# Kernel tuning notes

Measured on AMD Instinct MI355X. Metric: run time of the kernel, lower is better.

The kernel has to match this reference:

```python
import jax, jax.numpy as jnp
import numpy as np
from jax import lax

D = 1024      # input_dim
H = 4096      # hidden_dim (4*D)
E = 8         # num_experts
TOPK = 2      # sparse_top_k


def setup_inputs() -> dict:
    key = jax.random.key(0)
    ks = jax.random.split(key, 7)
    s = 0.02
    return {
        "x": jax.random.normal(ks[0], (2, 2048, D), dtype=jnp.float32),
        "W1": jax.random.normal(ks[1], (E, D, H), dtype=jnp.float32) * s,
        "b1": jnp.zeros((E, H), dtype=jnp.float32),
        "W2": jax.random.normal(ks[2], (E, H, D), dtype=jnp.float32) * s,
        "b2": jnp.zeros((E, D), dtype=jnp.float32),
        "Wr": jax.random.normal(ks[3], (D, E), dtype=jnp.float32) * s,
        "br": jnp.zeros((E,), dtype=jnp.float32),
    }


def reference(x, W1, b1, W2, b2, Wr, br):
    B, S, _ = x.shape
    xf = x.reshape(-1, D)                                  # [T, D]
    logits = xf @ Wr + br                                  # [T, E]
    # top-k threshold masking (keep logits >= k-th largest, else -inf)
    topv, _ = lax.top_k(logits, TOPK)                      # [T, k]
    thresh = topv[:, TOPK - 1:TOPK]                        # [T, 1]
    masked = jnp.where(logits >= thresh, logits, -jnp.inf)
    weights = jax.nn.softmax(masked, axis=-1)              # [T, E]
    # run ALL experts densely (faithful to reference), then weighted sum
    h = jax.nn.gelu(jnp.einsum('td,edh->eth', xf, W1) + b1[:, None, :],
                    approximate=False)                     # [E, T, H]
    expert_out = jnp.einsum('eth,ehd->etd', h, W2) + b2[:, None, :]  # [E, T, D]
    out = jnp.einsum('etd,te->td', expert_out, weights)    # [T, D]
    return out.reshape(B, S, D)
```

## Files before the change

### kernel.cpp

```cpp
#include <hip/hip_runtime.h>
#include <math.h>

typedef __bf16 bf16x8 __attribute__((ext_vector_type(8)));
typedef float f32x4 __attribute__((ext_vector_type(4)));

#define DDIM 1024
#define HDIM 4096
#define NE 8
#define TT 4096
#define CAP 9216

static const size_t OFF_CTRL   = 0;
static const size_t OFF_ROWMAP = 256;
static const size_t OFF_WROW   = OFF_ROWMAP + (size_t)CAP * 4;
static const size_t OFF_ROWPOS = OFF_WROW + (size_t)CAP * 4;
static const size_t OFF_TOKE   = OFF_ROWPOS + (size_t)TT * 2 * 4;
static const size_t OFF_TOKW   = OFF_TOKE + (size_t)TT * 2 * 4;
static const size_t OFF_XB     = OFF_TOKW + (size_t)TT * 2 * 4;
static const size_t OFF_W1T    = OFF_XB + (size_t)TT * DDIM * 2;
static const size_t OFF_W2T    = OFF_W1T + (size_t)NE * HDIM * DDIM * 2;
static const size_t OFF_H      = OFF_W2T + (size_t)NE * DDIM * HDIM * 2;
static const size_t OFF_PO     = OFF_H + (size_t)CAP * HDIM * 2;
static const size_t WS_NEED    = OFF_PO + (size_t)CAP * DDIM * 4;

__device__ __forceinline__ unsigned short f2bf(float f) {
  unsigned int u = __builtin_bit_cast(unsigned int, f);
  u = (u + 0x7FFFu + ((u >> 16) & 1u)) >> 16;
  return (unsigned short)u;
}

__device__ __forceinline__ void async16(void* lds, const void* g) {
  __builtin_amdgcn_global_load_lds(
      (__attribute__((address_space(1))) void*)g,
      (__attribute__((address_space(3))) void*)lds, 16, 0, 0);
}

__device__ __forceinline__ float gelu_exact(float v) {
  return 0.5f * v * (1.0f + erff(v * 0.70710678118654752f));
}

__global__ __launch_bounds__(256) void router_k(
    const float* __restrict__ x, const float* __restrict__ Wr, const float* __restrict__ br,
    unsigned short* __restrict__ xb, int* __restrict__ toke, float* __restrict__ tokw) {
  int tid = threadIdx.x, lane = tid & 63, wid = tid >> 6;
  int t = blockIdx.x * 4 + wid;
  const float* xr = x + (size_t)t * DDIM;
  float acc[NE];
#pragma unroll
  for (int e = 0; e < NE; ++e) acc[e] = 0.f;
#pragma unroll
  for (int it = 0; it < DDIM / 64; ++it) {
    int d = lane + it * 64;
    float xv = xr[d];
    xb[(size_t)t * DDIM + d] = f2bf(xv);
    const float4* w4 = (const float4*)(Wr + (size_t)d * NE);
    float4 wa = w4[0], wb = w4[1];
    acc[0] += xv * wa.x; acc[1] += xv * wa.y; acc[2] += xv * wa.z; acc[3] += xv * wa.w;
    acc[4] += xv * wb.x; acc[5] += xv * wb.y; acc[6] += xv * wb.z; acc[7] += xv * wb.w;
  }
#pragma unroll
  for (int e = 0; e < NE; ++e) {
#pragma unroll
    for (int s = 32; s > 0; s >>= 1) acc[e] += __shfl_xor(acc[e], s, 64);
  }
  if (lane == 0) {
    float l[NE];
#pragma unroll
    for (int e = 0; e < NE; ++e) l[e] = acc[e] + br[e];
    int i0 = 0; float m0 = l[0];
#pragma unroll
    for (int e = 1; e < NE; ++e) if (l[e] > m0) { m0 = l[e]; i0 = e; }
    int i1 = -1; float m1 = -3.4e38f;
#pragma unroll
    for (int e = 0; e < NE; ++e) if (e != i0 && l[e] > m1) { m1 = l[e]; i1 = e; }
    float e1 = expf(m1 - m0);
    float s = 1.f + e1;
    toke[2 * t] = i0;  toke[2 * t + 1] = i1;
    tokw[2 * t] = 1.f / s;  tokw[2 * t + 1] = e1 / s;
  }
}

__global__ __launch_bounds__(1024) void bin_k(
    const int* __restrict__ toke, const float* __restrict__ tokw,
    int* __restrict__ ctrl, int* __restrict__ rowmap,
    float* __restrict__ wrow, int* __restrict__ rowpos) {
  __shared__ int wcnt[16][8];
  __shared__ int wpre[16][8];
  __shared__ int pbase[9];
  __shared__ int ecnt[8];
  __shared__ int ebase[8];
  int tid = threadIdx.x, lane = tid & 63, w = tid >> 6;

  int myCnt = 0;
  for (int c = 0; c < 8; ++c) {
    int e = toke[c * 1024 + tid];
#pragma unroll
    for (int ee = 0; ee < 8; ++ee) {
      unsigned long long m = __ballot(e == ee);
      if (lane == ee) myCnt += (int)__popcll(m);
    }
  }
  if (lane < 8) wcnt[w][lane] = myCnt;
  __syncthreads();
  if (tid == 0) {
    int off = 0;
    for (int e = 0; e < 8; ++e) {
      int s = 0;
      for (int ww = 0; ww < 16; ++ww) s += wcnt[ww][e];
      ecnt[e] = s;
      pbase[e] = off;
      ebase[e] = off;
      ctrl[8 + e] = off;
      off += ((s + 127) >> 7) << 7;
    }
    pbase[8] = off;
    ctrl[16] = off;
  }
  __syncthreads();

  for (int e = 0; e < 8; ++e) {
    int start = pbase[e] + ecnt[e], end = pbase[e + 1];
    for (int r = start + tid; r < end; r += 1024) { rowmap[r] = 0; wrow[r] = 0.f; }
  }

  for (int c = 0; c < 8; ++c) {
    int slot = c * 1024 + tid;
    int e = toke[slot];
    unsigned long long mown = 0;
#pragma unroll
    for (int ee = 0; ee < 8; ++ee) {
      unsigned long long m = __ballot(e == ee);
      if (lane == ee) wcnt[w][ee] = (int)__popcll(m);
      if (e == ee) mown = m;
    }
    __syncthreads();
    if (tid < 128) {
      int ww = tid >> 3, ee = tid & 7;
      int s = 0;
      for (int p = 0; p < ww; ++p) s += wcnt[p][ee];
      wpre[ww][ee] = s;
    }
    __syncthreads();
    int rank = (int)__popcll(mown & ((1ull << lane) - 1ull));
    int r = ebase[e] + wpre[w][e] + rank;
    rowmap[r] = slot >> 1;
    wrow[r] = tokw[slot];
    rowpos[slot] = r;
    __syncthreads();
    if (tid < 8) {
      int s = 0;
      for (int ww = 0; ww < 16; ++ww) s += wcnt[ww][tid];
      ebase[tid] += s;
    }
    __syncthreads();
  }
}

__global__ __launch_bounds__(256) void convT_k(
    const float* __restrict__ src, unsigned short* __restrict__ dst, int K_, int N_) {
  __shared__ unsigned int lds32[64][33];
  int e = blockIdx.z;
  int kb = blockIdx.y << 6, nb = blockIdx.x << 6;
  int t = threadIdx.x;
  const float* s = src + (size_t)e * K_ * N_ + (size_t)kb * N_ + nb;
  int n0 = (t & 15) << 2;
#pragma unroll
  for (int i = 0; i < 2; ++i) {
    int k2 = (i << 4) + (t >> 4);
    float4 a = *(const float4*)(s + (size_t)(2 * k2) * N_ + n0);
    float4 b = *(const float4*)(s + (size_t)(2 * k2 + 1) * N_ + n0);
    lds32[n0 + 0][k2] = (unsigned)f2bf(a.x) | ((unsigned)f2bf(b.x) << 16);
    lds32[n0 + 1][k2] = (unsigned)f2bf(a.y) | ((unsigned)f2bf(b.y) << 16);
    lds32[n0 + 2][k2] = (unsigned)f2bf(a.z) | ((unsigned)f2bf(b.z) << 16);
    lds32[n0 + 3][k2] = (unsigned)f2bf(a.w) | ((unsigned)f2bf(b.w) << 16);
  }
  __syncthreads();
  unsigned short* dp = dst + (size_t)e * (size_t)N_ * K_ + (size_t)nb * K_ + kb;
  int n = t >> 2, c = t & 3;
  uint4 v0, v1;
  v0.x = lds32[n][(c << 2) + 0]; v0.y = lds32[n][(c << 2) + 1];
  v0.z = lds32[n][(c << 2) + 2]; v0.w = lds32[n][(c << 2) + 3];
  int c4 = (c + 4) << 2;
  v1.x = lds32[n][c4 + 0]; v1.y = lds32[n][c4 + 1];
  v1.z = lds32[n][c4 + 2]; v1.w = lds32[n][c4 + 3];
  *(uint4*)(dp + (size_t)n * K_ + (c << 3)) = v0;
  *(uint4*)(dp + (size_t)n * K_ + ((c + 4) << 3)) = v1;
}

template <int KTOT, int NTOT, bool GATHER, bool DOGELU, bool KSPLIT2>
__global__ __launch_bounds__(256, 2) void gemm_k(
    const unsigned short* __restrict__ A, const unsigned short* __restrict__ Bt,
    const int* __restrict__ ctrl, const int* __restrict__ rowmap,
    const float* __restrict__ wrow, const float* __restrict__ bias,
    unsigned short* __restrict__ outb, float* __restrict__ outf0, float* __restrict__ outf1) {
  __shared__ __align__(16) unsigned short Asm[128 * 64];
  __shared__ __align__(16) unsigned short Bsm[128 * 64];
  int zz = blockIdx.z;
  int e = KSPLIT2 ? (zz & 7) : zz;
  int ks = KSPLIT2 ? (zz >> 3) : 0;
  int off0 = ctrl[8 + e], off1 = ctrl[8 + e + 1];
  int row0 = off0 + (blockIdx.y << 7);
  if (row0 >= off1) return;
  int col0 = blockIdx.x << 7;
  int tid = threadIdx.x, lane = tid & 63, wid = tid >> 6;
  int wr = wid >> 1, wc = wid & 1;
  int kbeg = KSPLIT2 ? ks * (KTOT / 2) : 0;
  int kend = KSPLIT2 ? kbeg + (KTOT / 2) : KTOT;
  float* outf = (KSPLIT2 && ks) ? outf1 : outf0;

  const unsigned short* Asrc[4];
  const unsigned short* Bsrc[4];
#pragma unroll
  for (int c = 0; c < 4; ++c) {
    int ar = row0 + (c << 5) + (tid >> 3);
    size_t arow = GATHER ? (size_t)rowmap[ar] : (size_t)ar;
    Asrc[c] = A + arow * KTOT + ((tid & 7) << 3);
    int brw = col0 + (c << 5) + (tid >> 3);
    Bsrc[c] = Bt + ((size_t)e * NTOT + brw) * KTOT + ((tid & 7) << 3);
  }

  f32x4 acc[4][4];
#pragma unroll
  for (int m = 0; m < 4; ++m)
#pragma unroll
    for (int n = 0; n < 4; ++n) acc[m][n] = (f32x4){0.f, 0.f, 0.f, 0.f};

  int arow_rd = ((wr << 6) + (lane & 15)) << 6;
  int brow_rd = ((wc << 6) + (lane & 15)) << 6;
  int koff = (lane >> 4) << 3;
  char* AsmB = (char*)Asm;
  char* BsmB = (char*)Bsm;

  for (int k0 = kbeg; k0 < kend; k0 += 64) {
#pragma unroll
    for (int c = 0; c < 4; ++c) {
      async16(AsmB + ((c << 8) + (wid << 6)) * 16, Asrc[c] + k0);
      async16(BsmB + ((c << 8) + (wid << 6)) * 16, Bsrc[c] + k0);
    }
    __syncthreads();
#pragma unroll
    for (int kk = 0; kk < 64; kk += 32) {
      bf16x8 af[4], bfr[4];
#pragma unroll
      for (int m = 0; m < 4; ++m)
        af[m] = *(const bf16x8*)&Asm[arow_rd + (m << 10) + kk + koff];
#pragma unroll
      for (int n = 0; n < 4; ++n)
        bfr[n] = *(const bf16x8*)&Bsm[brow_rd + (n << 10) + kk + koff];
#pragma unroll
      for (int m = 0; m < 4; ++m)
#pragma unroll
        for (int n = 0; n < 4; ++n)
          acc[m][n] = __builtin_amdgcn_mfma_f32_16x16x32_bf16(af[m], bfr[n], acc[m][n], 0, 0, 0);
    }
    __syncthreads();
  }

  int r_b = (lane >> 4) << 2;
  int c_b = lane & 15;
  if (DOGELU) {
#pragma unroll
    for (int n = 0; n < 4; ++n) {
      int col = col0 + (wc << 6) + (n << 4) + c_b;
      float bv = bias[e * NTOT + col];
#pragma unroll
      for (int m = 0; m < 4; ++m) {
#pragma unroll
        for (int r = 0; r < 4; ++r) {
          int row = row0 + (wr << 6) + (m << 4) + r_b + r;
          outb[(size_t)row * NTOT + col] = f2bf(gelu_exact(acc[m][n][r] + bv));
        }
      }
    }
  } else {
#pragma unroll
    for (int n = 0; n < 4; ++n) {
      int col = col0 + (wc << 6) + (n << 4) + c_b;
      float bv = (KSPLIT2 && ks) ? 0.f : bias[e * NTOT + col];
#pragma unroll
      for (int m = 0; m < 4; ++m) {
#pragma unroll
        for (int r = 0; r < 4; ++r) {
          int row = row0 + (wr << 6) + (m << 4) + r_b + r;
          outf[(size_t)row * NTOT + col] = wrow[row] * (acc[m][n][r] + bv);
        }
      }
    }
  }
}

__global__ __launch_bounds__(256) void gather_k(
    const float* __restrict__ p0, const float* __restrict__ p1,
    const int* __restrict__ rowpos, float* __restrict__ out) {
  int t = blockIdx.x, d = threadIdx.x << 2;
  int r0 = rowpos[2 * t], r1 = rowpos[2 * t + 1];
  float4 a0 = *(const float4*)&p0[(size_t)r0 * DDIM + d];
  float4 a1 = *(const float4*)&p1[(size_t)r0 * DDIM + d];
  float4 b0 = *(const float4*)&p0[(size_t)r1 * DDIM + d];
  float4 b1 = *(const float4*)&p1[(size_t)r1 * DDIM + d];
  float4 o;
  o.x = (a0.x + a1.x) + (b0.x + b1.x);
  o.y = (a0.y + a1.y) + (b0.y + b1.y);
  o.z = (a0.z + a1.z) + (b0.z + b1.z);
  o.w = (a0.w + a1.w) + (b0.w + b1.w);
  *(float4*)&out[(size_t)t * DDIM + d] = o;
}

extern "C" void kernel_launch(void* const* d_in, const int* in_sizes, int n_in,
                              void* d_out, int out_size, void* d_ws, size_t ws_size,
                              hipStream_t stream) {
  const float* x  = (const float*)d_in[0];
  const float* W1 = (const float*)d_in[1];
  const float* b1 = (const float*)d_in[2];
  const float* W2 = (const float*)d_in[3];
  const float* b2 = (const float*)d_in[4];
  const float* Wr = (const float*)d_in[5];
  const float* br = (const float*)d_in[6];
  float* out = (float*)d_out;

  if (ws_size < WS_NEED) return;

  char* ws = (char*)d_ws;
  int* ctrl            = (int*)(ws + OFF_CTRL);
  int* rowmap          = (int*)(ws + OFF_ROWMAP);
  float* wrow          = (float*)(ws + OFF_WROW);
  int* rowpos          = (int*)(ws + OFF_ROWPOS);
  int* toke            = (int*)(ws + OFF_TOKE);
  float* tokw          = (float*)(ws + OFF_TOKW);
  unsigned short* xb   = (unsigned short*)(ws + OFF_XB);
  unsigned short* W1T  = (unsigned short*)(ws + OFF_W1T);
  unsigned short* W2T  = (unsigned short*)(ws + OFF_W2T);
  unsigned short* hbuf = (unsigned short*)(ws + OFF_H);
  float* pout          = (float*)(ws + OFF_PO);
  float* pout2         = (float*)(ws + OFF_W1T);

  router_k<<<TT / 4, 256, 0, stream>>>(x, Wr, br, xb, toke, tokw);
  bin_k<<<1, 1024, 0, stream>>>(toke, tokw, ctrl, rowmap, wrow, rowpos);

  convT_k<<<dim3(HDIM / 64, DDIM / 64, NE), 256, 0, stream>>>(W1, W1T, DDIM, HDIM);
  convT_k<<<dim3(DDIM / 64, HDIM / 64, NE), 256, 0, stream>>>(W2, W2T, HDIM, DDIM);

  gemm_k<DDIM, HDIM, true, true, false><<<dim3(HDIM / 128, 32, NE), 256, 0, stream>>>(
      xb, W1T, ctrl, rowmap, wrow, b1, hbuf, nullptr, nullptr);
  gemm_k<HDIM, DDIM, false, false, true><<<dim3(DDIM / 128, 32, NE * 2), 256, 0, stream>>>(
      hbuf, W2T, ctrl, rowmap, wrow, b2, nullptr, pout, pout2);

  gather_k<<<TT, 256, 0, stream>>>(pout, pout2, rowpos, out);
}
```

Baseline: 377.7 us.

## Store split-K partial outputs in bf16, vectorize router, raise GEMM occupancy

The second GEMM now writes its split-K partial outputs as bf16 instead of fp32, and the gather kernel converts them back to float before summing. This halves the partial-output write and read traffic and shrinks the workspace. The router loads x as float4 and stores bf16 x as ushort4, and the GEMM launch bound is raised to 4 blocks per CU, which may cap registers and cause spills. Rounding the partials to bf16 before the final sum adds precision loss.

```diff
diff --git a/kernel.cpp b/kernel.cpp
--- a/kernel.cpp
+++ b/kernel.cpp
@@ -21,12 +21,16 @@
 static const size_t OFF_W2T    = OFF_W1T + (size_t)NE * HDIM * DDIM * 2;
 static const size_t OFF_H      = OFF_W2T + (size_t)NE * DDIM * HDIM * 2;
 static const size_t OFF_PO     = OFF_H + (size_t)CAP * HDIM * 2;
-static const size_t WS_NEED    = OFF_PO + (size_t)CAP * DDIM * 4;
+static const size_t WS_NEED    = OFF_PO + (size_t)CAP * DDIM * 2;
 
 __device__ __forceinline__ unsigned short f2bf(float f) {
   unsigned int u = __builtin_bit_cast(unsigned int, f);
   u = (u + 0x7FFFu + ((u >> 16) & 1u)) >> 16;
   return (unsigned short)u;
+}
+
+__device__ __forceinline__ float bf2f(unsigned short s) {
+  return __builtin_bit_cast(float, (unsigned int)s << 16);
 }
 
 __device__ __forceinline__ void async16(void* lds, const void* g) {
@@ -49,14 +53,29 @@
 #pragma unroll
   for (int e = 0; e < NE; ++e) acc[e] = 0.f;
 #pragma unroll
-  for (int it = 0; it < DDIM / 64; ++it) {
-    int d = lane + it * 64;
-    float xv = xr[d];
-    xb[(size_t)t * DDIM + d] = f2bf(xv);
-    const float4* w4 = (const float4*)(Wr + (size_t)d * NE);
-    float4 wa = w4[0], wb = w4[1];
-    acc[0] += xv * wa.x; acc[1] += xv * wa.y; acc[2] += xv * wa.z; acc[3] += xv * wa.w;
-    acc[4] += xv * wb.x; acc[5] += xv * wb.y; acc[6] += xv * wb.z; acc[7] += xv * wb.w;
+  for (int it = 0; it < DDIM / 256; ++it) {
+    int d0 = it * 256 + lane * 4;
+    float4 xv = *(const float4*)(xr + d0);
+    ushort4 xs;
+    xs.x = f2bf(xv.x); xs.y = f2bf(xv.y); xs.z = f2bf(xv.z); xs.w = f2bf(xv.w);
+    *(ushort4*)(xb + (size_t)t * DDIM + d0) = xs;
+    const float4* w0 = (const float4*)(Wr + (size_t)(d0 + 0) * NE);
+    const float4* w1 = (const float4*)(Wr + (size_t)(d0 + 1) * NE);
+    const float4* w2 = (const float4*)(Wr + (size_t)(d0 + 2) * NE);
+    const float4* w3 = (const float4*)(Wr + (size_t)(d0 + 3) * NE);
+    float4 a, b;
+    a = w0[0]; b = w0[1];
+    acc[0] += xv.x * a.x; acc[1] += xv.x * a.y; acc[2] += xv.x * a.z; acc[3] += xv.x * a.w;
+    acc[4] += xv.x * b.x; acc[5] += xv.x * b.y; acc[6] += xv.x * b.z; acc[7] += xv.x * b.w;
+    a = w1[0]; b = w1[1];
+    acc[0] += xv.y * a.x; acc[1] += xv.y * a.y; acc[2] += xv.y * a.z; acc[3] += xv.y * a.w;
+    acc[4] += xv.y * b.x; acc[5] += xv.y * b.y; acc[6] += xv.y * b.z; acc[7] += xv.y * b.w;
+    a = w2[0]; b = w2[1];
+    acc[0] += xv.z * a.x; acc[1] += xv.z * a.y; acc[2] += xv.z * a.z; acc[3] += xv.z * a.w;
+    acc[4] += xv.z * b.x; acc[5] += xv.z * b.y; acc[6] += xv.z * b.z; acc[7] += xv.z * b.w;
+    a = w3[0]; b = w3[1];
+    acc[0] += xv.w * a.x; acc[1] += xv.w * a.y; acc[2] += xv.w * a.z; acc[3] += xv.w * a.w;
+    acc[4] += xv.w * b.x; acc[5] += xv.w * b.y; acc[6] += xv.w * b.z; acc[7] += xv.w * b.w;
   }
 #pragma unroll
   for (int e = 0; e < NE; ++e) {
@@ -188,11 +207,11 @@
 }
 
 template <int KTOT, int NTOT, bool GATHER, bool DOGELU, bool KSPLIT2>
-__global__ __launch_bounds__(256, 2) void gemm_k(
+__global__ __launch_bounds__(256, 4) void gemm_k(
     const unsigned short* __restrict__ A, const unsigned short* __restrict__ Bt,
     const int* __restrict__ ctrl, const int* __restrict__ rowmap,
     const float* __restrict__ wrow, const float* __restrict__ bias,
-    unsigned short* __restrict__ outb, float* __restrict__ outf0, float* __restrict__ outf1) {
+    unsigned short* __restrict__ out0, unsigned short* __restrict__ out1) {
   __shared__ __align__(16) unsigned short Asm[128 * 64];
   __shared__ __align__(16) unsigned short Bsm[128 * 64];
   int zz = blockIdx.z;
@@ -206,7 +225,7 @@
   int wr = wid >> 1, wc = wid & 1;
   int kbeg = KSPLIT2 ? ks * (KTOT / 2) : 0;
   int kend = KSPLIT2 ? kbeg + (KTOT / 2) : KTOT;
-  float* outf = (KSPLIT2 && ks) ? outf1 : outf0;
+  unsigned short* outp = (KSPLIT2 && ks) ? out1 : out0;
 
   const unsigned short* Asrc[4];
   const unsigned short* Bsrc[4];
@@ -268,7 +287,7 @@
 #pragma unroll
         for (int r = 0; r < 4; ++r) {
           int row = row0 + (wr << 6) + (m << 4) + r_b + r;
-          outb[(size_t)row * NTOT + col] = f2bf(gelu_exact(acc[m][n][r] + bv));
+          out0[(size_t)row * NTOT + col] = f2bf(gelu_exact(acc[m][n][r] + bv));
         }
       }
     }
@@ -282,7 +301,7 @@
 #pragma unroll
         for (int r = 0; r < 4; ++r) {
           int row = row0 + (wr << 6) + (m << 4) + r_b + r;
-          outf[(size_t)row * NTOT + col] = wrow[row] * (acc[m][n][r] + bv);
+          outp[(size_t)row * NTOT + col] = f2bf(wrow[row] * (acc[m][n][r] + bv));
         }
       }
     }
@@ -290,19 +309,19 @@
 }
 
 __global__ __launch_bounds__(256) void gather_k(
-    const float* __restrict__ p0, const float* __restrict__ p1,
+    const unsigned short* __restrict__ p0, const unsigned short* __restrict__ p1,
     const int* __restrict__ rowpos, float* __restrict__ out) {
   int t = blockIdx.x, d = threadIdx.x << 2;
   int r0 = rowpos[2 * t], r1 = rowpos[2 * t + 1];
-  float4 a0 = *(const float4*)&p0[(size_t)r0 * DDIM + d];
-  float4 a1 = *(const float4*)&p1[(size_t)r0 * DDIM + d];
-  float4 b0 = *(const float4*)&p0[(size_t)r1 * DDIM + d];
-  float4 b1 = *(const float4*)&p1[(size_t)r1 * DDIM + d];
+  ushort4 a0 = *(const ushort4*)&p0[(size_t)r0 * DDIM + d];
+  ushort4 a1 = *(const ushort4*)&p1[(size_t)r0 * DDIM + d];
+  ushort4 b0 = *(const ushort4*)&p0[(size_t)r1 * DDIM + d];
+  ushort4 b1 = *(const ushort4*)&p1[(size_t)r1 * DDIM + d];
   float4 o;
-  o.x = (a0.x + a1.x) + (b0.x + b1.x);
-  o.y = (a0.y + a1.y) + (b0.y + b1.y);
-  o.z = (a0.z + a1.z) + (b0.z + b1.z);
-  o.w = (a0.w + a1.w) + (b0.w + b1.w);
+  o.x = (bf2f(a0.x) + bf2f(a1.x)) + (bf2f(b0.x) + bf2f(b1.x));
+  o.y = (bf2f(a0.y) + bf2f(a1.y)) + (bf2f(b0.y) + bf2f(b1.y));
+  o.z = (bf2f(a0.z) + bf2f(a1.z)) + (bf2f(b0.z) + bf2f(b1.z));
+  o.w = (bf2f(a0.w) + bf2f(a1.w)) + (bf2f(b0.w) + bf2f(b1.w));
   *(float4*)&out[(size_t)t * DDIM + d] = o;
 }
 
@@ -331,8 +350,8 @@
   unsigned short* W1T  = (unsigned short*)(ws + OFF_W1T);
   unsigned short* W2T  = (unsigned short*)(ws + OFF_W2T);
   unsigned short* hbuf = (unsigned short*)(ws + OFF_H);
-  float* pout          = (float*)(ws + OFF_PO);
-  float* pout2         = (float*)(ws + OFF_W1T);
+  unsigned short* pout = (unsigned short*)(ws + OFF_PO);
+  unsigned short* pout2 = (unsigned short*)(ws + OFF_W1T);
 
   router_k<<<TT / 4, 256, 0, stream>>>(x, Wr, br, xb, toke, tokw);
   bin_k<<<1, 1024, 0, stream>>>(toke, tokw, ctrl, rowmap, wrow, rowpos);
@@ -341,9 +360,9 @@
   convT_k<<<dim3(DDIM / 64, HDIM / 64, NE), 256, 0, stream>>>(W2, W2T, HDIM, DDIM);
 
   gemm_k<DDIM, HDIM, true, true, false><<<dim3(HDIM / 128, 32, NE), 256, 0, stream>>>(
-      xb, W1T, ctrl, rowmap, wrow, b1, hbuf, nullptr, nullptr);
+      xb, W1T, ctrl, rowmap, wrow, b1, hbuf, nullptr);
   gemm_k<HDIM, DDIM, false, false, true><<<dim3(DDIM / 128, 32, NE * 2), 256, 0, stream>>>(
-      hbuf, W2T, ctrl, rowmap, wrow, b2, nullptr, pout, pout2);
+      hbuf, W2T, ctrl, rowmap, wrow, b2, pout, pout2);
 
   gather_k<<<TT, 256, 0, stream>>>(pout, pout2, rowpos, out);
 }
```

New measurement: 426.6 us. 1.13x slower.
